# Performance work log

Measured on AMD Instinct MI355X. Metric: run time of the kernel, lower is better.

Reference implementation:

```python
import jax, jax.numpy as jnp
import numpy as np

SEQ, B, CIN, H, K = 2048, 16, 512, 512, 2

def setup_inputs() -> dict:
    key = jax.random.key(0)
    k1, k2, k3 = jax.random.split(key, 3)
    x = jax.random.normal(k1, (SEQ, B, CIN), dtype=jnp.float32)
    W = jax.random.normal(k2, (3 * H, CIN, K), dtype=jnp.float32) * (1.0 / np.sqrt(CIN * K))
    b = jax.random.normal(k3, (3 * H,), dtype=jnp.float32) * 0.01
    return {"x": x, "W": W, "b": b}

def _qrnn_fo(x, W, b):
    # x: (T, B, Cin) -> conv input (B, Cin, T), causal left pad of K-1 zeros
    xb = jnp.transpose(x, (1, 2, 0))
    g = jax.lax.conv_general_dilated(
        xb, W, window_strides=(1,), padding=[(K - 1, 0)],
        dimension_numbers=("NCH", "OIH", "NCH"))
    g = g + b[None, :, None]
    g = jnp.transpose(g, (2, 0, 1))  # (T, B, 3H)
    zg, fg, og = jnp.split(g, 3, axis=-1)
    z = jnp.tanh(zg)
    f = jax.nn.sigmoid(fg)
    o = jax.nn.sigmoid(og)

    def step(c, gates_t):
        zt, ft, ot = gates_t
        c = ft * c + (1.0 - ft) * zt
        h = c * ot
        return c, h

    c0 = jnp.zeros((B, H), dtype=x.dtype)
    c_last, hs = jax.lax.scan(step, c0, (z, f, o))
    return hs, c_last

def reference(x, W, b):
    hs, c_last = _qrnn_fo(x, W, b)
    h_last = hs[-1]
    return hs, h_last[None, :], c_last[None, :]
```

## Files before the change

kernel.cpp:

```cpp
#include <hip/hip_runtime.h>

#define SEQ   2048
#define BATCH 16
#define CINCH 512
#define HDIM  512
#define NDIM  1536
#define TBM   (SEQ*BATCH)
#define KRED  1024
#define NCH   32
#define CHL   64
#define NCOL  8192

typedef unsigned short ushort_t;
typedef __bf16 bf16x8 __attribute__((ext_vector_type(8)));
typedef unsigned short u16x8 __attribute__((ext_vector_type(8)));
typedef float f32x4 __attribute__((ext_vector_type(4)));

__device__ __forceinline__ float bf2f(ushort_t u) {
    return __uint_as_float(((unsigned int)u) << 16);
}
__device__ __forceinline__ ushort_t f2bf(float x) {
    unsigned int u = __float_as_uint(x);
    unsigned int r = u + 0x7fffu + ((u >> 16) & 1u);
    return (ushort_t)(r >> 16);
}

__global__ void cast_x_kernel(const float* __restrict__ x, ushort_t* __restrict__ xb) {
    int i = blockIdx.x * 256 + threadIdx.x;
    int e = i * 4;
    ushort4 r;
    if (e < BATCH * CINCH) {
        r.x = 0; r.y = 0; r.z = 0; r.w = 0;
    } else {
        float4 v = *(const float4*)(x + (e - BATCH * CINCH));
        r.x = f2bf(v.x); r.y = f2bf(v.y); r.z = f2bf(v.z); r.w = f2bf(v.w);
    }
    *(ushort4*)(xb + e) = r;
}

__global__ void repack_w_kernel(const float* __restrict__ W, ushort_t* __restrict__ wb) {
    int i = blockIdx.x * 256 + threadIdx.x;
    int o  = i >> 10;
    int r  = i & 1023;
    int k  = r >> 9;
    int ci = r & 511;
    wb[i] = f2bf(W[o * 1024 + ci * 2 + k]);
}

__device__ __forceinline__ void load_lds_16B(const ushort_t* g, ushort_t* l) {
    auto* gp = reinterpret_cast<const __attribute__((address_space(1))) unsigned int*>(
        reinterpret_cast<uintptr_t>(g));
    auto* lp = reinterpret_cast<__attribute__((address_space(3))) unsigned int*>(
        reinterpret_cast<uintptr_t>(l));
    __builtin_amdgcn_global_load_lds(gp, lp, 16, 0, 0);
}

__device__ __forceinline__ bf16x8 frag(const ushort_t* buf, int row, int cb) {
    return __builtin_bit_cast(bf16x8,
        *(const u16x8*)(&buf[row * 64 + ((cb ^ (row & 7)) * 8)]));
}

#define PHASE_BAR() do { __builtin_amdgcn_s_barrier(); asm volatile("" ::: "memory"); } while (0)

__global__ __launch_bounds__(512, 2) void gemm_gates_kernel(
    const ushort_t* __restrict__ xb, const ushort_t* __restrict__ wb,
    const float* __restrict__ bias,
    ushort_t* __restrict__ zb, ushort_t* __restrict__ fb, ushort_t* __restrict__ ob) {

    extern __shared__ ushort_t smem[];

    const int tid  = threadIdx.x;
    const int w    = tid >> 6;
    const int lane = tid & 63;
    const int quad = lane >> 4;
    const int l15  = lane & 15;
    const int wm   = w >> 2;
    const int wn   = w & 3;

    const int wg    = (blockIdx.x & 7) * 96 + (blockIdx.x >> 3);
    const int mBase = (wg / 6) * 256;
    const int nBase = (wg % 6) * 256;

    const int r0    = tid >> 3;
    const int cbd   = (tid & 7) ^ (r0 & 7);
    const int wbase = w * 8;

    auto stageA = [&](ushort_t* dst, int u) {
        const long aoff = (u < 8) ? (long)u * 64 : 8192L + (long)(u - 8) * 64;
#pragma unroll
        for (int ra = 0; ra < 4; ++ra) {
            load_lds_16B(xb + (long)(mBase + ra * 64 + r0) * 512 + aoff + cbd * 8,
                         dst + (ra * 64 + wbase) * 64);
        }
    };
    auto stageB = [&](ushort_t* dst, int u) {
        const long koff = (long)u * 64;
#pragma unroll
        for (int ra = 0; ra < 4; ++ra) {
            load_lds_16B(wb + (long)(nBase + ra * 64 + r0) * 1024 + koff + cbd * 8,
                         dst + (ra * 64 + wbase) * 64);
        }
    };

    f32x4 acc[8][4];
#pragma unroll
    for (int i = 0; i < 8; ++i)
#pragma unroll
        for (int j = 0; j < 4; ++j)
            acc[i][j] = (f32x4){0.f, 0.f, 0.f, 0.f};

    stageA(smem, 0);
    stageB(smem + 32768, 0);
    stageB(smem + 49152, 1);
    asm volatile("s_waitcnt vmcnt(4)" ::: "memory");
    PHASE_BAR();

    int cur = 0;
    for (int t = 0; t < 16; ++t) {
        const ushort_t* cA = smem + cur * 16384;
        const ushort_t* cB = smem + 32768 + cur * 16384;
        bf16x8 a[4], b[4];

#pragma unroll
        for (int mt = 0; mt < 4; ++mt) a[mt] = frag(cA, wm * 128 + mt * 16 + l15, quad);
#pragma unroll
        for (int nt = 0; nt < 4; ++nt) b[nt] = frag(cB, wn * 64 + nt * 16 + l15, quad);
        if (t < 15) stageA(smem + (cur ^ 1) * 16384, t + 1);
        __builtin_amdgcn_s_setprio(1);
#pragma unroll
        for (int mt = 0; mt < 4; ++mt)
#pragma unroll
            for (int nt = 0; nt < 4; ++nt)
                acc[mt][nt] = __builtin_amdgcn_mfma_f32_16x16x32_bf16(a[mt], b[nt], acc[mt][nt], 0, 0, 0);
        __builtin_amdgcn_s_setprio(0);
        PHASE_BAR();

#pragma unroll
        for (int mt = 0; mt < 4; ++mt) a[mt] = frag(cA, wm * 128 + (mt + 4) * 16 + l15, quad);
        __builtin_amdgcn_s_setprio(1);
#pragma unroll
        for (int mt = 0; mt < 4; ++mt)
#pragma unroll
            for (int nt = 0; nt < 4; ++nt)
                acc[mt + 4][nt] = __builtin_amdgcn_mfma_f32_16x16x32_bf16(a[mt], b[nt], acc[mt + 4][nt], 0, 0, 0);
        __builtin_amdgcn_s_setprio(0);
        PHASE_BAR();

#pragma unroll
        for (int mt = 0; mt < 4; ++mt) a[mt] = frag(cA, wm * 128 + mt * 16 + l15, 4 + quad);
#pragma unroll
        for (int nt = 0; nt < 4; ++nt) b[nt] = frag(cB, wn * 64 + nt * 16 + l15, 4 + quad);
        __builtin_amdgcn_s_setprio(1);
#pragma unroll
        for (int mt = 0; mt < 4; ++mt)
#pragma unroll
            for (int nt = 0; nt < 4; ++nt)
                acc[mt][nt] = __builtin_amdgcn_mfma_f32_16x16x32_bf16(a[mt], b[nt], acc[mt][nt], 0, 0, 0);
        __builtin_amdgcn_s_setprio(0);
        PHASE_BAR();

#pragma unroll
        for (int mt = 0; mt < 4; ++mt) a[mt] = frag(cA, wm * 128 + (mt + 4) * 16 + l15, 4 + quad);
        __builtin_amdgcn_s_setprio(1);
#pragma unroll
        for (int mt = 0; mt < 4; ++mt)
#pragma unroll
            for (int nt = 0; nt < 4; ++nt)
                acc[mt + 4][nt] = __builtin_amdgcn_mfma_f32_16x16x32_bf16(a[mt], b[nt], acc[mt + 4][nt], 0, 0, 0);
        __builtin_amdgcn_s_setprio(0);
        if (t < 14) {
            stageB(smem + 32768 + cur * 16384, t + 2);
            asm volatile("s_waitcnt vmcnt(4)" ::: "memory");
        } else {
            asm volatile("s_waitcnt vmcnt(0)" ::: "memory");
        }
        PHASE_BAR();
        cur ^= 1;
    }

    const int gate = nBase >> 9;
    const int hb   = nBase & 511;

#pragma unroll
    for (int nt = 0; nt < 4; ++nt) {
        const int n_local = wn * 64 + nt * 16 + l15;
        const float bv = bias[nBase + n_local];
#pragma unroll
        for (int mt = 0; mt < 8; ++mt) {
#pragma unroll
            for (int r = 0; r < 4; ++r) {
                const int m_local = wm * 128 + mt * 16 + quad * 4 + r;
                float g = acc[mt][nt][r] + bv;
                float av;
                if (gate == 0) {
                    float e = __expf(-2.f * fabsf(g));
                    float tt = (1.f - e) / (1.f + e);
                    av = copysignf(tt, g);
                } else {
                    av = 1.f / (1.f + __expf(-g));
                }
                const int phys = ((n_local >> 3) ^ (m_local & 7)) * 8 + (n_local & 7);
                smem[m_local * 256 + phys] = f2bf(av);
            }
        }
    }
    __syncthreads();

    ushort_t* outp = (gate == 0) ? zb : (gate == 1) ? fb : ob;
    const int lb    = tid & 31;
    const int mrow0 = tid >> 5;
#pragma unroll
    for (int s = 0; s < 16; ++s) {
        const int m_local = s * 16 + mrow0;
        u16x8 v = *(const u16x8*)(&smem[m_local * 256 + ((lb ^ (m_local & 7)) * 8)]);
        *(u16x8*)(outp + (long)(mBase + m_local) * 512 + hb + lb * 8) = v;
    }
}

__device__ __forceinline__ void scan_step(float z, float f, float& A, float& Bv) {
    Bv = f * Bv + (1.f - f) * z;
    A *= f;
}

__global__ __launch_bounds__(256) void scan_compose(
    const ushort_t* __restrict__ zb, const ushort_t* __restrict__ fb,
    float* __restrict__ Acomp, float* __restrict__ Bcomp) {
    const int cg  = (blockIdx.x & 7) * 256 + threadIdx.x;
    const int ch  = blockIdx.x >> 3;
    const int col = cg * 4;
    const long base = (long)ch * CHL * NCOL + col;
    float Ax = 1.f, Ay = 1.f, Az = 1.f, Aw = 1.f;
    float Bx = 0.f, By = 0.f, Bz = 0.f, Bw = 0.f;
    const int U = 8;
    for (int w0 = 0; w0 < CHL; w0 += U) {
        ushort4 zr[U], fr[U];
#pragma unroll
        for (int u = 0; u < U; ++u) {
            const long idx = base + (long)(w0 + u) * NCOL;
            zr[u] = *(const ushort4*)(zb + idx);
            fr[u] = *(const ushort4*)(fb + idx);
        }
#pragma unroll
        for (int u = 0; u < U; ++u) {
            scan_step(bf2f(zr[u].x), bf2f(fr[u].x), Ax, Bx);
            scan_step(bf2f(zr[u].y), bf2f(fr[u].y), Ay, By);
            scan_step(bf2f(zr[u].z), bf2f(fr[u].z), Az, Bz);
            scan_step(bf2f(zr[u].w), bf2f(fr[u].w), Aw, Bw);
        }
    }
    *(float4*)(Acomp + (long)ch * NCOL + col) = make_float4(Ax, Ay, Az, Aw);
    *(float4*)(Bcomp + (long)ch * NCOL + col) = make_float4(Bx, By, Bz, Bw);
}

__global__ void scan_prefix(const float* __restrict__ Acomp,
                            const float* __restrict__ Bcomp,
                            float* __restrict__ Cin) {
    const int col = blockIdx.x * 256 + threadIdx.x;
    float c = 0.f;
#pragma unroll 4
    for (int ch = 0; ch < NCH; ++ch) {
        Cin[ch * NCOL + col] = c;
        c = Acomp[ch * NCOL + col] * c + Bcomp[ch * NCOL + col];
    }
}

__global__ __launch_bounds__(256) void scan_apply(
    const ushort_t* __restrict__ zb, const ushort_t* __restrict__ fb,
    const ushort_t* __restrict__ ob, const float* __restrict__ Cin,
    float* __restrict__ out) {
    const int cg  = (blockIdx.x & 7) * 256 + threadIdx.x;
    const int ch  = blockIdx.x >> 3;
    const int col = cg * 4;
    const long base = (long)ch * CHL * NCOL + col;
    float4 c0 = *(const float4*)(Cin + (long)ch * NCOL + col);
    float cx = c0.x, cy = c0.y, cz = c0.z, cw = c0.w;
    float hx = 0.f, hy = 0.f, hz = 0.f, hw = 0.f;
    const int U = 8;
    for (int w0 = 0; w0 < CHL; w0 += U) {
        ushort4 zr[U], fr[U], orr[U];
#pragma unroll
        for (int u = 0; u < U; ++u) {
            const long idx = base + (long)(w0 + u) * NCOL;
            zr[u]  = *(const ushort4*)(zb + idx);
            fr[u]  = *(const ushort4*)(fb + idx);
            orr[u] = *(const ushort4*)(ob + idx);
        }
#pragma unroll
        for (int u = 0; u < U; ++u) {
            float f, z;
            f = bf2f(fr[u].x); z = bf2f(zr[u].x); cx = f * cx + (1.f - f) * z; hx = cx * bf2f(orr[u].x);
            f = bf2f(fr[u].y); z = bf2f(zr[u].y); cy = f * cy + (1.f - f) * z; hy = cy * bf2f(orr[u].y);
            f = bf2f(fr[u].z); z = bf2f(zr[u].z); cz = f * cz + (1.f - f) * z; hz = cz * bf2f(orr[u].z);
            f = bf2f(fr[u].w); z = bf2f(zr[u].w); cw = f * cw + (1.f - f) * z; hw = cw * bf2f(orr[u].w);
            *(float4*)(out + base + (long)(w0 + u) * NCOL) = make_float4(hx, hy, hz, hw);
        }
    }
    if (ch == NCH - 1) {
        *(float4*)(out + (long)SEQ * NCOL + col)        = make_float4(hx, hy, hz, hw);
        *(float4*)(out + (long)SEQ * NCOL + NCOL + col) = make_float4(cx, cy, cz, cw);
    }
}

extern "C" void kernel_launch(void* const* d_in, const int* in_sizes, int n_in,
                              void* d_out, int out_size, void* d_ws, size_t ws_size,
                              hipStream_t stream) {
    const float* x  = (const float*)d_in[0];
    const float* W  = (const float*)d_in[1];
    const float* bi = (const float*)d_in[2];
    float* out = (float*)d_out;

    char* ws = (char*)d_ws;
    const size_t xbN = (size_t)(TBM + BATCH) * CINCH;
    const size_t wbN = (size_t)NDIM * KRED;
    const size_t gN  = (size_t)TBM * HDIM;
    ushort_t* xb = (ushort_t*)ws;
    ushort_t* wb = (ushort_t*)(ws + xbN * 2);
    ushort_t* zb = (ushort_t*)(ws + xbN * 2 + wbN * 2);
    ushort_t* fb = zb + gN;
    ushort_t* ob = fb + gN;
    float* Acomp = (float*)ws;
    float* Bcomp = Acomp + NCH * NCOL;
    float* Cin   = Bcomp + NCH * NCOL;

    static bool s_attr_set = false;
    if (!s_attr_set) {
        (void)hipFuncSetAttribute(reinterpret_cast<const void*>(&gemm_gates_kernel),
                                  hipFuncAttributeMaxDynamicSharedMemorySize, 131072);
        s_attr_set = true;
    }

    cast_x_kernel<<<16392, 256, 0, stream>>>(x, xb);
    repack_w_kernel<<<6144, 256, 0, stream>>>(W, wb);
    gemm_gates_kernel<<<dim3(768), 512, 131072, stream>>>(xb, wb, bi, zb, fb, ob);
    scan_compose<<<NCH * 8, 256, 0, stream>>>(zb, fb, Acomp, Bcomp);
    scan_prefix<<<NCOL / 256, 256, 0, stream>>>(Acomp, Bcomp, Cin);
    scan_apply<<<NCH * 8, 256, 0, stream>>>(zb, fb, ob, Cin, out);
}
```

Before: 291.2 us.

## Load GEMM B operand directly from global into registers, shrink LDS to A only

The gates GEMM no longer stages weight tiles in LDS. Each wave loads its B fragments straight from global memory into registers and double-buffers them across k-halves. LDS now holds only the double-buffered A tiles as a 64 KB static array, and the epilogue is split into two 128-row halves that reuse that smaller buffer. The aim is to cut LDS traffic and footprint and drop barriers per iteration, so that two 512-thread blocks fit per CU. In exchange, weight fragments come through uncoalesced per-lane global reads whose latency the MFMA work must hide.

New measurement: 360.5 us. +23.8%, slower.

```diff
diff --git a/kernel.cpp b/kernel.cpp
--- a/kernel.cpp
+++ b/kernel.cpp
@@ -60,6 +60,10 @@
         *(const u16x8*)(&buf[row * 64 + ((cb ^ (row & 7)) * 8)]));
 }
 
+__device__ __forceinline__ bf16x8 bload(const ushort_t* p) {
+    return __builtin_bit_cast(bf16x8, *(const u16x8*)(p));
+}
+
 #define PHASE_BAR() do { __builtin_amdgcn_s_barrier(); asm volatile("" ::: "memory"); } while (0)
 
 __global__ __launch_bounds__(512, 2) void gemm_gates_kernel(
@@ -67,7 +71,7 @@
     const float* __restrict__ bias,
     ushort_t* __restrict__ zb, ushort_t* __restrict__ fb, ushort_t* __restrict__ ob) {
 
-    extern __shared__ ushort_t smem[];
+    __shared__ ushort_t smem[2 * 256 * 64];
 
     const int tid  = threadIdx.x;
     const int w    = tid >> 6;
@@ -93,14 +97,8 @@
                          dst + (ra * 64 + wbase) * 64);
         }
     };
-    auto stageB = [&](ushort_t* dst, int u) {
-        const long koff = (long)u * 64;
-#pragma unroll
-        for (int ra = 0; ra < 4; ++ra) {
-            load_lds_16B(wb + (long)(nBase + ra * 64 + r0) * 1024 + koff + cbd * 8,
-                         dst + (ra * 64 + wbase) * 64);
-        }
-    };
+
+    const long bro = (long)(nBase + wn * 64 + l15) * 1024 + (long)quad * 8;
 
     f32x4 acc[8][4];
 #pragma unroll
@@ -109,111 +107,98 @@
         for (int j = 0; j < 4; ++j)
             acc[i][j] = (f32x4){0.f, 0.f, 0.f, 0.f};
 
+    bf16x8 b0[4], b1[4];
+
     stageA(smem, 0);
-    stageB(smem + 32768, 0);
-    stageB(smem + 49152, 1);
+#pragma unroll
+    for (int nt = 0; nt < 4; ++nt)
+        b0[nt] = bload(wb + bro + nt * 16384);
     asm volatile("s_waitcnt vmcnt(4)" ::: "memory");
     PHASE_BAR();
 
-    int cur = 0;
     for (int t = 0; t < 16; ++t) {
-        const ushort_t* cA = smem + cur * 16384;
-        const ushort_t* cB = smem + 32768 + cur * 16384;
-        bf16x8 a[4], b[4];
-
-#pragma unroll
-        for (int mt = 0; mt < 4; ++mt) a[mt] = frag(cA, wm * 128 + mt * 16 + l15, quad);
-#pragma unroll
-        for (int nt = 0; nt < 4; ++nt) b[nt] = frag(cB, wn * 64 + nt * 16 + l15, quad);
-        if (t < 15) stageA(smem + (cur ^ 1) * 16384, t + 1);
+        const ushort_t* cA = smem + (t & 1) * 16384;
+        const int tn = (t + 1) & 15;
+        bf16x8 a[8];
+
+#pragma unroll
+        for (int nt = 0; nt < 4; ++nt)
+            b1[nt] = bload(wb + bro + nt * 16384 + 32 + (long)t * 64);
+
+#pragma unroll
+        for (int mt = 0; mt < 8; ++mt) a[mt] = frag(cA, wm * 128 + mt * 16 + l15, quad);
         __builtin_amdgcn_s_setprio(1);
 #pragma unroll
-        for (int mt = 0; mt < 4; ++mt)
+        for (int mt = 0; mt < 8; ++mt)
 #pragma unroll
             for (int nt = 0; nt < 4; ++nt)
-                acc[mt][nt] = __builtin_amdgcn_mfma_f32_16x16x32_bf16(a[mt], b[nt], acc[mt][nt], 0, 0, 0);
+                acc[mt][nt] = __builtin_amdgcn_mfma_f32_16x16x32_bf16(a[mt], b0[nt], acc[mt][nt], 0, 0, 0);
         __builtin_amdgcn_s_setprio(0);
+
+        stageA(smem + ((t + 1) & 1) * 16384, tn);
+#pragma unroll
+        for (int nt = 0; nt < 4; ++nt)
+            b0[nt] = bload(wb + bro + nt * 16384 + (long)tn * 64);
+
+#pragma unroll
+        for (int mt = 0; mt < 8; ++mt) a[mt] = frag(cA, wm * 128 + mt * 16 + l15, 4 + quad);
+        __builtin_amdgcn_s_setprio(1);
+#pragma unroll
+        for (int mt = 0; mt < 8; ++mt)
+#pragma unroll
+            for (int nt = 0; nt < 4; ++nt)
+                acc[mt][nt] = __builtin_amdgcn_mfma_f32_16x16x32_bf16(a[mt], b1[nt], acc[mt][nt], 0, 0, 0);
+        __builtin_amdgcn_s_setprio(0);
+
+        asm volatile("s_waitcnt vmcnt(4)" ::: "memory");
         PHASE_BAR();
-
-#pragma unroll
-        for (int mt = 0; mt < 4; ++mt) a[mt] = frag(cA, wm * 128 + (mt + 4) * 16 + l15, quad);
-        __builtin_amdgcn_s_setprio(1);
-#pragma unroll
-        for (int mt = 0; mt < 4; ++mt)
-#pragma unroll
-            for (int nt = 0; nt < 4; ++nt)
-                acc[mt + 4][nt] = __builtin_amdgcn_mfma_f32_16x16x32_bf16(a[mt], b[nt], acc[mt + 4][nt], 0, 0, 0);
-        __builtin_amdgcn_s_setprio(0);
-        PHASE_BAR();
-
-#pragma unroll
-        for (int mt = 0; mt < 4; ++mt) a[mt] = frag(cA, wm * 128 + mt * 16 + l15, 4 + quad);
-#pragma unroll
-        for (int nt = 0; nt < 4; ++nt) b[nt] = frag(cB, wn * 64 + nt * 16 + l15, 4 + quad);
-        __builtin_amdgcn_s_setprio(1);
-#pragma unroll
-        for (int mt = 0; mt < 4; ++mt)
-#pragma unroll
-            for (int nt = 0; nt < 4; ++nt)
-                acc[mt][nt] = __builtin_amdgcn_mfma_f32_16x16x32_bf16(a[mt], b[nt], acc[mt][nt], 0, 0, 0);
-        __builtin_amdgcn_s_setprio(0);
-        PHASE_BAR();
-
-#pragma unroll
-        for (int mt = 0; mt < 4; ++mt) a[mt] = frag(cA, wm * 128 + (mt + 4) * 16 + l15, 4 + quad);
-        __builtin_amdgcn_s_setprio(1);
-#pragma unroll
-        for (int mt = 0; mt < 4; ++mt)
-#pragma unroll
-            for (int nt = 0; nt < 4; ++nt)
-                acc[mt + 4][nt] = __builtin_amdgcn_mfma_f32_16x16x32_bf16(a[mt], b[nt], acc[mt + 4][nt], 0, 0, 0);
-        __builtin_amdgcn_s_setprio(0);
-        if (t < 14) {
-            stageB(smem + 32768 + cur * 16384, t + 2);
-            asm volatile("s_waitcnt vmcnt(4)" ::: "memory");
-        } else {
-            asm volatile("s_waitcnt vmcnt(0)" ::: "memory");
-        }
-        PHASE_BAR();
-        cur ^= 1;
-    }
+    }
+
+    asm volatile("s_waitcnt vmcnt(0)" ::: "memory");
+    __syncthreads();
 
     const int gate = nBase >> 9;
     const int hb   = nBase & 511;
-
-#pragma unroll
-    for (int nt = 0; nt < 4; ++nt) {
-        const int n_local = wn * 64 + nt * 16 + l15;
-        const float bv = bias[nBase + n_local];
-#pragma unroll
-        for (int mt = 0; mt < 8; ++mt) {
-#pragma unroll
-            for (int r = 0; r < 4; ++r) {
-                const int m_local = wm * 128 + mt * 16 + quad * 4 + r;
-                float g = acc[mt][nt][r] + bv;
-                float av;
-                if (gate == 0) {
-                    float e = __expf(-2.f * fabsf(g));
-                    float tt = (1.f - e) / (1.f + e);
-                    av = copysignf(tt, g);
-                } else {
-                    av = 1.f / (1.f + __expf(-g));
-                }
-                const int phys = ((n_local >> 3) ^ (m_local & 7)) * 8 + (n_local & 7);
-                smem[m_local * 256 + phys] = f2bf(av);
-            }
-        }
-    }
-    __syncthreads();
-
     ushort_t* outp = (gate == 0) ? zb : (gate == 1) ? fb : ob;
     const int lb    = tid & 31;
     const int mrow0 = tid >> 5;
-#pragma unroll
-    for (int s = 0; s < 16; ++s) {
-        const int m_local = s * 16 + mrow0;
-        u16x8 v = *(const u16x8*)(&smem[m_local * 256 + ((lb ^ (m_local & 7)) * 8)]);
-        *(u16x8*)(outp + (long)(mBase + m_local) * 512 + hb + lb * 8) = v;
+
+#pragma unroll
+    for (int h = 0; h < 2; ++h) {
+        if (wm == h) {
+#pragma unroll
+            for (int nt = 0; nt < 4; ++nt) {
+                const int n_local = wn * 64 + nt * 16 + l15;
+                const float bv = bias[nBase + n_local];
+#pragma unroll
+                for (int mt = 0; mt < 8; ++mt) {
+#pragma unroll
+                    for (int r = 0; r < 4; ++r) {
+                        const int mrow = mt * 16 + quad * 4 + r;
+                        float g = acc[mt][nt][r] + bv;
+                        float av;
+                        if (gate == 0) {
+                            float e = __expf(-2.f * fabsf(g));
+                            float tt = (1.f - e) / (1.f + e);
+                            av = copysignf(tt, g);
+                        } else {
+                            av = 1.f / (1.f + __expf(-g));
+                        }
+                        const int phys = ((n_local >> 3) ^ (mrow & 7)) * 8 + (n_local & 7);
+                        smem[mrow * 256 + phys] = f2bf(av);
+                    }
+                }
+            }
+        }
+        __syncthreads();
+#pragma unroll
+        for (int s = 0; s < 8; ++s) {
+            const int mr = s * 16 + mrow0;
+            const int m_local = h * 128 + mr;
+            u16x8 v = *(const u16x8*)(&smem[mr * 256 + ((lb ^ (mr & 7)) * 8)]);
+            *(u16x8*)(outp + (long)(mBase + m_local) * 512 + hb + lb * 8) = v;
+        }
+        __syncthreads();
     }
 }
 
@@ -322,16 +307,9 @@
     float* Bcomp = Acomp + NCH * NCOL;
     float* Cin   = Bcomp + NCH * NCOL;
 
-    static bool s_attr_set = false;
-    if (!s_attr_set) {
-        (void)hipFuncSetAttribute(reinterpret_cast<const void*>(&gemm_gates_kernel),
-                                  hipFuncAttributeMaxDynamicSharedMemorySize, 131072);
-        s_attr_set = true;
-    }
-
     cast_x_kernel<<<16392, 256, 0, stream>>>(x, xb);
     repack_w_kernel<<<6144, 256, 0, stream>>>(W, wb);
-    gemm_gates_kernel<<<dim3(768), 512, 131072, stream>>>(xb, wb, bi, zb, fb, ob);
+    gemm_gates_kernel<<<dim3(768), 512, 0, stream>>>(xb, wb, bi, zb, fb, ob);
     scan_compose<<<NCH * 8, 256, 0, stream>>>(zb, fb, Acomp, Bcomp);
     scan_prefix<<<NCOL / 256, 256, 0, stream>>>(Acomp, Bcomp, Cin);
     scan_apply<<<NCH * 8, 256, 0, stream>>>(zb, fb, ob, Cin, out);
```
